# Kernel optimization log

Hardware: AMD Instinct MI355X
Metric: run time of the kernel (lower is better)

The kernel has to match this reference:

```python
import jax, jax.numpy as jnp
import numpy as np

B, T, H, NUM_LAYERS = 8, 4096, 1024, 2


def _log_g(x):
    # log of g(x) = where(x>=0, x+0.5, sigmoid(x)), computed stably in log space
    return jnp.where(x >= 0.0, jnp.log(jax.nn.relu(x) + 0.5), -jax.nn.softplus(-x))


def _heinsen_scan(log_coeffs, log_values):
    # parallel scan for h_t = a_t * h_{t-1} + b_t in log space, along time axis 1
    a_star = jnp.cumsum(log_coeffs, axis=1)                       # [B,T,H]
    return jnp.exp(a_star + jax.lax.cumlogsumexp(log_values - a_star, axis=1))


def setup_inputs() -> dict:
    key = jax.random.key(0)
    k0, k1, k2 = jax.random.split(key, 3)
    scale = 1.0 / np.sqrt(H)
    return {
        "h": jax.random.normal(k0, (B, T, H), dtype=jnp.float32),
        "W0": jax.random.normal(k1, (H, 3 * H), dtype=jnp.float32) * scale,
        "W1": jax.random.normal(k2, (H, 3 * H), dtype=jnp.float32) * scale,
    }


def reference(h, W0, W1):
    for W in (W0, W1):
        z = jnp.einsum('bth,hk->btk', h, W)                       # [B,T,3H]
        hidden, gate, proj = jnp.split(z, 3, axis=-1)             # each [B,T,H]
        log_coeffs = -jax.nn.softplus(gate)                       # log(1 - sigmoid(gate))
        log_values = -jax.nn.softplus(-gate) + _log_g(hidden)     # log(sigmoid(gate)*g(hidden))
        out = _heinsen_scan(log_coeffs, log_values)               # [B,T,H]
        g = jax.nn.sigmoid(proj)
        h = g * out + (1.0 - g) * h                               # highway gate
    return h
```

## Files before the change

kernel.cpp:

```cpp
#include <hip/hip_runtime.h>

#define Bc 8
#define Td 4096
#define Hd 1024
#define N3 3072
#define Md (Bc*Td)
#define Kd Hd

#define NC 128
#define CL (Td/NC)

#define BM2 256
#define BN2 256
#define BK2 64
#define NT (Kd/BK2)
#define NSEG (4*NT)

typedef _Float16 half8 __attribute__((ext_vector_type(8)));
typedef _Float16 half4v __attribute__((ext_vector_type(4)));
typedef float floatx4 __attribute__((ext_vector_type(4)));

typedef __attribute__((address_space(3))) unsigned int lds_u32;
typedef __attribute__((address_space(1))) const unsigned int glob_u32;

__device__ __forceinline__ void async_lds16(const void* g, void* l) {
    __builtin_amdgcn_global_load_lds((glob_u32*)g, (lds_u32*)l, 16, 0, 0);
}

__device__ __forceinline__ float sigm(float x) {
    return 1.0f / (1.0f + __expf(-x));
}
__device__ __forceinline__ float gfun(float x) {
    float e = __expf(-fabsf(x));
    return (x >= 0.0f) ? (x + 0.5f) : e / (1.0f + e);
}

__global__ void cvt16(const float4* __restrict__ x, half4v* __restrict__ y, int n4) {
    int i = blockIdx.x * blockDim.x + threadIdx.x;
    if (i < n4) {
        float4 v = x[i];
        half4v o;
        o[0] = (_Float16)v.x; o[1] = (_Float16)v.y;
        o[2] = (_Float16)v.z; o[3] = (_Float16)v.w;
        y[i] = o;
    }
}

__global__ void wtrans(const float* __restrict__ W, _Float16* __restrict__ Wt) {
    __shared__ float t[32][33];
    int n0 = blockIdx.x * 32, k0 = blockIdx.y * 32;
    int tx = threadIdx.x, ty = threadIdx.y;
    t[ty][tx] = W[(size_t)(k0 + ty) * N3 + n0 + tx];
    __syncthreads();
    Wt[(size_t)(n0 + ty) * Kd + k0 + tx] = (_Float16)t[tx][ty];
}

__global__ __launch_bounds__(512, 2) void gemm_f16_bt_256(
    const _Float16* __restrict__ A,
    const _Float16* __restrict__ Bt,
    _Float16* __restrict__ C)
{
    __shared__ _Float16 lds[2][4][128 * 64];

    const int tid  = threadIdx.x;
    const int wave = tid >> 6;
    const int lane = tid & 63;

    const int bid = blockIdx.x;
    const int swz = (bid & 7) * (1536 / 8) + (bid >> 3);
    const int by  = swz / 12;
    const int bx  = swz - by * 12;
    const int bm  = by * BM2;
    const int bn  = bx * BN2;

    const int wm   = (wave >> 2) * 128;
    const int wn   = (wave & 3) * 64;
    const int quad = lane >> 4;
    const int lr   = lane & 15;
    const int aslot = wm ? 3 : 0;
    const int bslot = (wn >= 128) ? 2 : 1;
    const int bro   = wn & 127;

    floatx4 acc[8][4];
#pragma unroll
    for (int i = 0; i < 8; ++i)
#pragma unroll
        for (int j = 0; j < 4; ++j) { floatx4 z = {0.f,0.f,0.f,0.f}; acc[i][j] = z; }

    auto stage_seg = [&](int seg) {
        const int tt    = seg >> 2;
        const int b     = seg & 3;
        const int sel   = tt & 1;
        const int k0    = tt * BK2;
        const bool isA  = (b & 1);
        const int rbase = (b >= 2) ? 128 : 0;
        const int slot  = (b < 2) ? (1 - b) : b;
        const _Float16* src = isA ? A : Bt;
        const int g0    = (isA ? bm : bn) + rbase;
#pragma unroll
        for (int r = 0; r < 2; ++r) {
            int rl = r * 64 + wave * 8 + (lane >> 3);
            int kc = ((lane & 7) ^ (rl & 7)) << 3;
            const _Float16* g = src + (size_t)(g0 + rl) * Kd + (k0 + kc);
            char* l = (char*)&lds[sel][slot][0] + (r * 64 + wave * 8) * 128;
            async_lds16(g, l);
        }
    };

    auto dsA = [&](int sel, int ih, half8 (&af)[4][2]) {
#pragma unroll
        for (int i = 0; i < 4; ++i) {
            int row = (ih * 4 + i) * 16 + lr;
#pragma unroll
            for (int ks = 0; ks < 2; ++ks) {
                int ck = ((ks * 4 + quad) ^ (row & 7)) << 3;
                af[i][ks] = *(const half8*)&lds[sel][aslot][row * 64 + ck];
            }
        }
    };
    auto dsB = [&](int sel, int jh, half8 (&bf)[2][2]) {
#pragma unroll
        for (int j = 0; j < 2; ++j) {
            int row = bro + (jh * 2 + j) * 16 + lr;
#pragma unroll
            for (int ks = 0; ks < 2; ++ks) {
                int ck = ((ks * 4 + quad) ^ (row & 7)) << 3;
                bf[j][ks] = *(const half8*)&lds[sel][bslot][row * 64 + ck];
            }
        }
    };
    auto mmac = [&](int ih, int jh, half8 (&af)[4][2], half8 (&bf)[2][2]) {
        __builtin_amdgcn_sched_barrier(0);
        __builtin_amdgcn_s_setprio(1);
#pragma unroll
        for (int i = 0; i < 4; ++i)
#pragma unroll
            for (int j = 0; j < 2; ++j)
#pragma unroll
                for (int ks = 0; ks < 2; ++ks)
                    acc[ih * 4 + i][jh * 2 + j] =
                        __builtin_amdgcn_mfma_f32_16x16x32_f16(
                            af[i][ks], bf[j][ks],
                            acc[ih * 4 + i][jh * 2 + j], 0, 0, 0);
        __builtin_amdgcn_s_setprio(0);
        __builtin_amdgcn_sched_barrier(0);
    };

    half8 af[4][2], bf0[2][2], bf1[2][2];

    for (int s = 0; s < 6; ++s) stage_seg(s);
    asm volatile("s_waitcnt vmcnt(4)" ::: "memory");
    asm volatile("s_barrier" ::: "memory");

    for (int kt = 0; kt < NT; ++kt) {
        const int sel = kt & 1;
        const int p = kt * 4;
        dsA(sel, 0, af); dsB(sel, 0, bf0);
        if (p + 6 < NSEG) stage_seg(p + 6);
        asm volatile("s_barrier" ::: "memory");
        mmac(0, 0, af, bf0);
        asm volatile("s_waitcnt lgkmcnt(0)" ::: "memory");
        asm volatile("s_barrier" ::: "memory");
        dsB(sel, 1, bf1);
        if (p + 7 < NSEG) stage_seg(p + 7);
        asm volatile("s_barrier" ::: "memory");
        mmac(0, 1, af, bf1);
        asm volatile("s_waitcnt lgkmcnt(0)" ::: "memory");
        asm volatile("s_barrier" ::: "memory");
        dsA(sel, 1, af);
        if (p + 8 < NSEG) stage_seg(p + 8);
        asm volatile("s_barrier" ::: "memory");
        mmac(1, 0, af, bf0);
        asm volatile("s_waitcnt lgkmcnt(0)" ::: "memory");
        asm volatile("s_barrier" ::: "memory");
        if (p + 9 < NSEG) stage_seg(p + 9);
        mmac(1, 1, af, bf1);
        if (kt < NT - 2) {
            asm volatile("s_waitcnt vmcnt(4)" ::: "memory");
            asm volatile("s_barrier" ::: "memory");
        } else if (kt == NT - 2) {
            asm volatile("s_waitcnt vmcnt(0)" ::: "memory");
            asm volatile("s_barrier" ::: "memory");
        }
    }

#pragma unroll
    for (int i = 0; i < 8; ++i) {
#pragma unroll
        for (int j = 0; j < 4; ++j) {
            int row0 = bm + wm + i * 16 + quad * 4;
            int col  = bn + wn + j * 16 + lr;
#pragma unroll
            for (int r = 0; r < 4; ++r)
                C[(size_t)(row0 + r) * N3 + col] = (_Float16)acc[i][j][r];
        }
    }
}

__global__ __launch_bounds__(256) void scan_phase1(
    const _Float16* __restrict__ Z, float* __restrict__ cA, float* __restrict__ cB)
{
    int ch = threadIdx.x * 4;
    int c  = blockIdx.y;
    int b  = blockIdx.z;
    const _Float16* zp = Z + ((size_t)(b * Td + c * CL)) * N3 + ch;
    float Ap[4] = {1.f, 1.f, 1.f, 1.f};
    float Bv[4] = {0.f, 0.f, 0.f, 0.f};
#pragma unroll 4
    for (int t = 0; t < CL; ++t) {
        half4v h4 = *(const half4v*)(zp);
        half4v g4 = *(const half4v*)(zp + Hd);
#pragma unroll
        for (int i = 0; i < 4; ++i) {
            float sg = sigm((float)g4[i]);
            float at = 1.0f - sg;
            float bt = sg * gfun((float)h4[i]);
            Ap[i] *= at;
            Bv[i] = fmaf(at, Bv[i], bt);
        }
        zp += N3;
    }
    size_t o = ((size_t)b * NC + c) * Hd + ch;
    *(float4*)&cA[o] = make_float4(Ap[0], Ap[1], Ap[2], Ap[3]);
    *(float4*)&cB[o] = make_float4(Bv[0], Bv[1], Bv[2], Bv[3]);
}

__global__ void scan_phase2(const float* __restrict__ cA, float* __restrict__ cB)
{
    int u = (blockIdx.x * 256 + threadIdx.x) * 4;
    int b = u >> 10, ch = u & 1023;
    float4 s = make_float4(0.f, 0.f, 0.f, 0.f);
    for (int c = 0; c < NC; ++c) {
        size_t o = ((size_t)b * NC + c) * Hd + ch;
        float4 a = *(const float4*)&cA[o];
        float4 v = *(const float4*)&cB[o];
        *(float4*)&cB[o] = s;
        s.x = fmaf(a.x, s.x, v.x);
        s.y = fmaf(a.y, s.y, v.y);
        s.z = fmaf(a.z, s.z, v.z);
        s.w = fmaf(a.w, s.w, v.w);
    }
}

__global__ __launch_bounds__(256) void scan_phase3(
    const _Float16* __restrict__ Z, const float* __restrict__ cS,
    const float* __restrict__ hin32, const _Float16* __restrict__ hin16,
    float* __restrict__ hout32, _Float16* __restrict__ hout16)
{
    int ch = threadIdx.x * 4;
    int c  = blockIdx.y;
    int b  = blockIdx.z;
    float s[4];
    {
        float4 s4 = *(const float4*)&cS[((size_t)b * NC + c) * Hd + ch];
        s[0] = s4.x; s[1] = s4.y; s[2] = s4.z; s[3] = s4.w;
    }
    const _Float16* zp = Z + ((size_t)(b * Td + c * CL)) * N3 + ch;
    size_t ho = ((size_t)(b * Td + c * CL)) * Hd + ch;
#pragma unroll 2
    for (int t = 0; t < CL; ++t) {
        half4v h4 = *(const half4v*)(zp);
        half4v g4 = *(const half4v*)(zp + Hd);
        half4v p4 = *(const half4v*)(zp + 2 * Hd);
        float hi[4];
        if (hin32) {
            float4 v = *(const float4*)&hin32[ho];
            hi[0] = v.x; hi[1] = v.y; hi[2] = v.z; hi[3] = v.w;
        } else {
            half4v v = *(const half4v*)&hin16[ho];
#pragma unroll
            for (int i = 0; i < 4; ++i) hi[i] = (float)v[i];
        }
        float o[4];
#pragma unroll
        for (int i = 0; i < 4; ++i) {
            float sg = sigm((float)g4[i]);
            float at = 1.0f - sg;
            s[i] = fmaf(at, s[i], sg * gfun((float)h4[i]));
            float gg = sigm((float)p4[i]);
            o[i] = fmaf(gg, s[i] - hi[i], hi[i]);
        }
        if (hout32) *(float4*)&hout32[ho] = make_float4(o[0], o[1], o[2], o[3]);
        if (hout16) {
            half4v v;
#pragma unroll
            for (int i = 0; i < 4; ++i) v[i] = (_Float16)o[i];
            *(half4v*)&hout16[ho] = v;
        }
        zp += N3; ho += Hd;
    }
}

extern "C" void kernel_launch(void* const* d_in, const int* in_sizes, int n_in,
                              void* d_out, int out_size, void* d_ws, size_t ws_size,
                              hipStream_t stream) {
    const float* h  = (const float*)d_in[0];
    const float* W0 = (const float*)d_in[1];
    const float* W1 = (const float*)d_in[2];
    float* out = (float*)d_out;

    char* ws = (char*)d_ws;
    _Float16* Z    = (_Float16*)ws; ws += (size_t)Md * N3 * 2;
    _Float16* Hbf  = (_Float16*)ws; ws += (size_t)Md * Kd * 2;
    _Float16* Wt   = (_Float16*)ws; ws += (size_t)N3 * Kd * 2;
    float* cA   = (float*)ws; ws += (size_t)Bc * NC * Hd * 4;
    float* cB   = (float*)ws; ws += (size_t)Bc * NC * Hd * 4;

    {
        int n4 = Md * Kd / 4;
        cvt16<<<n4 / 256, 256, 0, stream>>>((const float4*)h, (half4v*)Hbf, n4);
    }

    for (int l = 0; l < 2; ++l) {
        const float* W = l ? W1 : W0;

        wtrans<<<dim3(N3 / 32, Kd / 32), dim3(32, 32), 0, stream>>>(W, Wt);
        gemm_f16_bt_256<<<dim3((Md / BM2) * (N3 / BN2)), 512, 0, stream>>>(Hbf, Wt, Z);
        scan_phase1<<<dim3(1, NC, Bc), 256, 0, stream>>>(Z, cA, cB);
        scan_phase2<<<(Bc * Hd / 4) / 256, 256, 0, stream>>>(cA, cB);
        if (l == 0) {
            scan_phase3<<<dim3(1, NC, Bc), 256, 0, stream>>>(
                Z, cB, h, nullptr, nullptr, Hbf);
        } else {
            scan_phase3<<<dim3(1, NC, Bc), 256, 0, stream>>>(
                Z, cB, nullptr, Hbf, out, nullptr);
        }
    }
}
```

Before: 922.3 us.

## Parallelize chunk-carry scan and precompute GEMM load addresses

The chunk-carry scan (phase 2) changes from a sequential loop over 128 chunks per thread, with only 8 blocks, into a Hillis-Steele parallel scan in shared memory with one thread per chunk and 2048 blocks. This targets the latency-bound serial pass, at the cost of extra shared-memory traffic and barriers. The GEMM now precomputes per-row global load pointers, fully unrolls its prologue and main K loop, and drops one LDS waitcnt between MFMA phases to cut address arithmetic and stalls. Removing that waitcnt leans on the barrier and the compiler to order LDS reads before the MFMAs, which carries some correctness risk.

```diff
diff --git a/kernel.cpp b/kernel.cpp
--- a/kernel.cpp
+++ b/kernel.cpp
@@ -87,21 +87,26 @@
 #pragma unroll
         for (int j = 0; j < 4; ++j) { floatx4 z = {0.f,0.f,0.f,0.f}; acc[i][j] = z; }
 
+    const int rl0 = wave * 8 + (lane >> 3);
+    const int kc  = (((lane & 7) ^ (lane >> 3)) << 3);
+    const _Float16* gA[4];
+    const _Float16* gB[4];
+#pragma unroll
+    for (int q = 0; q < 4; ++q) {
+        gA[q] = A  + (size_t)(bm + q * 64 + rl0) * Kd + kc;
+        gB[q] = Bt + (size_t)(bn + q * 64 + rl0) * Kd + kc;
+    }
+
     auto stage_seg = [&](int seg) {
         const int tt    = seg >> 2;
         const int b     = seg & 3;
         const int sel   = tt & 1;
-        const int k0    = tt * BK2;
         const bool isA  = (b & 1);
-        const int rbase = (b >= 2) ? 128 : 0;
+        const int qb    = (b >= 2) ? 2 : 0;
         const int slot  = (b < 2) ? (1 - b) : b;
-        const _Float16* src = isA ? A : Bt;
-        const int g0    = (isA ? bm : bn) + rbase;
 #pragma unroll
         for (int r = 0; r < 2; ++r) {
-            int rl = r * 64 + wave * 8 + (lane >> 3);
-            int kc = ((lane & 7) ^ (rl & 7)) << 3;
-            const _Float16* g = src + (size_t)(g0 + rl) * Kd + (k0 + kc);
+            const _Float16* g = (isA ? gA[qb + r] : gB[qb + r]) + tt * BK2;
             char* l = (char*)&lds[sel][slot][0] + (r * 64 + wave * 8) * 128;
             async_lds16(g, l);
         }
@@ -148,10 +153,12 @@
 
     half8 af[4][2], bf0[2][2], bf1[2][2];
 
+#pragma unroll
     for (int s = 0; s < 6; ++s) stage_seg(s);
     asm volatile("s_waitcnt vmcnt(4)" ::: "memory");
     asm volatile("s_barrier" ::: "memory");
 
+#pragma unroll
     for (int kt = 0; kt < NT; ++kt) {
         const int sel = kt & 1;
         const int p = kt * 4;
@@ -159,7 +166,6 @@
         if (p + 6 < NSEG) stage_seg(p + 6);
         asm volatile("s_barrier" ::: "memory");
         mmac(0, 0, af, bf0);
-        asm volatile("s_waitcnt lgkmcnt(0)" ::: "memory");
         asm volatile("s_barrier" ::: "memory");
         dsB(sel, 1, bf1);
         if (p + 7 < NSEG) stage_seg(p + 7);
@@ -225,21 +231,40 @@
     *(float4*)&cB[o] = make_float4(Bv[0], Bv[1], Bv[2], Bv[3]);
 }
 
-__global__ void scan_phase2(const float* __restrict__ cA, float* __restrict__ cB)
+__global__ __launch_bounds__(128) void scan_phase2(
+    const float* __restrict__ cA, float* __restrict__ cB)
 {
-    int u = (blockIdx.x * 256 + threadIdx.x) * 4;
-    int b = u >> 10, ch = u & 1023;
-    float4 s = make_float4(0.f, 0.f, 0.f, 0.f);
-    for (int c = 0; c < NC; ++c) {
-        size_t o = ((size_t)b * NC + c) * Hd + ch;
-        float4 a = *(const float4*)&cA[o];
-        float4 v = *(const float4*)&cB[o];
-        *(float4*)&cB[o] = s;
-        s.x = fmaf(a.x, s.x, v.x);
-        s.y = fmaf(a.y, s.y, v.y);
-        s.z = fmaf(a.z, s.z, v.z);
-        s.w = fmaf(a.w, s.w, v.w);
-    }
+    const int c   = threadIdx.x;
+    const int chg = blockIdx.x;
+    const int b   = blockIdx.y;
+    const size_t o = ((size_t)b * NC + c) * Hd + chg * 4;
+    float4 a4 = *(const float4*)&cA[o];
+    float4 v4 = *(const float4*)&cB[o];
+    float a[4] = {a4.x, a4.y, a4.z, a4.w};
+    float v[4] = {v4.x, v4.y, v4.z, v4.w};
+    __shared__ float sA[4][NC], sV[4][NC];
+#pragma unroll
+    for (int d = 1; d < NC; d <<= 1) {
+#pragma unroll
+        for (int i = 0; i < 4; ++i) { sA[i][c] = a[i]; sV[i][c] = v[i]; }
+        __syncthreads();
+        if (c >= d) {
+#pragma unroll
+            for (int i = 0; i < 4; ++i) {
+                float ao = sA[i][c - d], vo = sV[i][c - d];
+                v[i] = fmaf(a[i], vo, v[i]);
+                a[i] *= ao;
+            }
+        }
+        __syncthreads();
+    }
+#pragma unroll
+    for (int i = 0; i < 4; ++i) sV[i][c] = v[i];
+    __syncthreads();
+    float4 out;
+    if (c == 0) out = make_float4(0.f, 0.f, 0.f, 0.f);
+    else        out = make_float4(sV[0][c-1], sV[1][c-1], sV[2][c-1], sV[3][c-1]);
+    *(float4*)&cB[o] = out;
 }
 
 __global__ __launch_bounds__(256) void scan_phase3(
@@ -317,7 +342,7 @@
         wtrans<<<dim3(N3 / 32, Kd / 32), dim3(32, 32), 0, stream>>>(W, Wt);
         gemm_f16_bt_256<<<dim3((Md / BM2) * (N3 / BN2)), 512, 0, stream>>>(Hbf, Wt, Z);
         scan_phase1<<<dim3(1, NC, Bc), 256, 0, stream>>>(Z, cA, cB);
-        scan_phase2<<<(Bc * Hd / 4) / 256, 256, 0, stream>>>(cA, cB);
+        scan_phase2<<<dim3(Hd / 4, Bc), 128, 0, stream>>>(cA, cB);
         if (l == 0) {
             scan_phase3<<<dim3(1, NC, Bc), 256, 0, stream>>>(
                 Z, cB, h, nullptr, nullptr, Hbf);
```

Result: no change. 906.1 us (-1.8%).
